# Kernel optimization log

Measured on AMD Instinct MI355X. Metric: run time of the kernel, lower is better.

## Reference

```python
import jax, jax.numpy as jnp
import numpy as np
from functools import partial


def conv2d(x, w, b, pad):
    # x: [B,C,H,W], w: [O,I,kh,kw]
    out = jax.lax.conv_general_dilated(
        x, w, window_strides=(1, 1), padding=[(pad, pad), (pad, pad)],
        dimension_numbers=("NCHW", "OIHW", "NCHW"))
    return out + b[None, :, None, None]


def maxpool3x3_s1(x):
    return jax.lax.reduce_window(
        x, -jnp.inf, jax.lax.max, (1, 1, 3, 3), (1, 1, 1, 1),
        padding=((0, 0), (0, 0), (1, 1), (1, 1)))


def bilinear_sample(img, y, x):
    # img: [B,C,H,W]; y, x: [B,H,W] float sample coords. Zero outside bounds.
    def one(im, yy, xx):  # im [C,H,W]
        H, W = im.shape[1], im.shape[2]
        y0 = jnp.floor(yy)
        x0 = jnp.floor(xx)
        wy = yy - y0
        wx = xx - x0
        y0i = y0.astype(jnp.int32)
        x0i = x0.astype(jnp.int32)

        def g(yi, xi):
            valid = (yi >= 0) & (yi < H) & (xi >= 0) & (xi < W)
            yc = jnp.clip(yi, 0, H - 1)
            xc = jnp.clip(xi, 0, W - 1)
            return im[:, yc, xc] * valid[None].astype(im.dtype)

        return (g(y0i, x0i) * ((1 - wy) * (1 - wx))[None]
                + g(y0i, x0i + 1) * ((1 - wy) * wx)[None]
                + g(y0i + 1, x0i) * (wy * (1 - wx))[None]
                + g(y0i + 1, x0i + 1) * (wy * wx)[None])

    return jax.vmap(one)(img, y, x)


def deform_conv2d(x, offset, weight, bias, k, pad):
    # torchvision-style: offset [B, 2*k*k, H, W], pairs are (dy, dx) in
    # row-major kernel order. stride=1, dilation=1.
    B, C, H, W = x.shape
    off = offset.reshape(B, k * k, 2, H, W)
    hh = jnp.arange(H, dtype=x.dtype)[None, :, None]  # [1,H,1]
    ww = jnp.arange(W, dtype=x.dtype)[None, None, :]  # [1,1,W]
    out = jnp.zeros((B, weight.shape[0], H, W), x.dtype)
    for t in range(k * k):
        i, j = t // k, t % k
        y = hh + (i - pad) + off[:, t, 0]  # [B,H,W]
        xc = ww + (j - pad) + off[:, t, 1]
        s = bilinear_sample(x, y, xc)      # [B,C,H,W]
        out = out + jnp.einsum("bchw,oc->bohw", s, weight[:, :, i, j])
    return out + bias[None, :, None, None]


def _mk(key, shape, scale=0.05):
    return jax.random.normal(key, shape, dtype=jnp.float32) * scale


def setup_inputs() -> dict:
    key = jax.random.key(0)
    ks = jax.random.split(key, 20)
    C = 512
    Cb = C // 4  # 128
    B, H, W = 8, 64, 64
    return {
        "x": jax.random.normal(ks[0], (B, C, H, W), dtype=jnp.float32),
        "w_b1": _mk(ks[1], (Cb, C, 1, 1)), "b_b1": jnp.zeros((Cb,), jnp.float32),
        "w_b21": _mk(ks[2], (Cb, C, 1, 1)), "b_b21": jnp.zeros((Cb,), jnp.float32),
        "w_off2": _mk(ks[3], (18, Cb, 3, 3), 0.01), "b_off2": jnp.zeros((18,), jnp.float32),
        "w_ddc2": _mk(ks[4], (Cb, Cb, 3, 3)), "b_ddc2": jnp.zeros((Cb,), jnp.float32),
        "w_b31": _mk(ks[5], (Cb, C, 1, 1)), "b_b31": jnp.zeros((Cb,), jnp.float32),
        "w_off3": _mk(ks[6], (50, Cb, 5, 5), 0.01), "b_off3": jnp.zeros((50,), jnp.float32),
        "w_ddc3": _mk(ks[7], (Cb, Cb, 5, 5)), "b_ddc3": jnp.zeros((Cb,), jnp.float32),
        "w_b4": _mk(ks[8], (Cb, C, 1, 1)), "b_b4": jnp.zeros((Cb,), jnp.float32),
        "w_cc": _mk(ks[9], (C, Cb * 4, 1, 1)), "b_cc": jnp.zeros((C,), jnp.float32),
    }


def reference(x, w_b1, b_b1, w_b21, b_b21, w_off2, b_off2, w_ddc2, b_ddc2,
              w_b31, b_b31, w_off3, b_off3, w_ddc3, b_ddc3, w_b4, b_b4,
              w_cc, b_cc):
    b1 = conv2d(x, w_b1, b_b1, 0)

    b2i = conv2d(x, w_b21, b_b21, 0)
    off2 = conv2d(b2i, w_off2, b_off2, 1)
    b2 = deform_conv2d(b2i, off2, w_ddc2, b_ddc2, k=3, pad=1)

    b3i = conv2d(x, w_b31, b_b31, 0)
    off3 = conv2d(b3i, w_off3, b_off3, 2)
    b3 = deform_conv2d(b3i, off3, w_ddc3, b_ddc3, k=5, pad=2)

    b4 = conv2d(maxpool3x3_s1(x), w_b4, b_b4, 0)

    cat = jnp.concatenate([b1, b2, b3, b4], axis=1) * x
    fused = conv2d(cat, w_cc, b_cc, 0)
    return x + jax.nn.sigmoid(fused)
```

## Files before the change

### kernel.cpp

```cpp
#include <hip/hip_runtime.h>
#include <math.h>

#define HW 4096
typedef short short8 __attribute__((ext_vector_type(8)));
typedef float floatx4 __attribute__((ext_vector_type(4)));

#define O_XBT   0ull
#define O_PXB   33554432ull
#define O_CATB  67108864ull
#define O_WPB   100663296ull
#define O_W4B   101056512ull
#define O_WCCB  101187584ull
#define O_WD2T  101711872ull
#define O_WD3T  102006784ull
#define O_WO2T  102825984ull
#define O_WO3T  102973440ull
#define O_T2B   33554432ull
#define O_T3B   41943040ull
#define O_OFF2  50331648ull
#define O_OFF3  52690944ull

__device__ __forceinline__ unsigned short f2b(float f) {
    union { float f; unsigned u; } v; v.f = f;
    unsigned r = v.u + 0x7FFFu + ((v.u >> 16) & 1u);
    return (unsigned short)(r >> 16);
}
__device__ __forceinline__ float lou(unsigned u) {
    union { unsigned u; float f; } v; v.u = u << 16; return v.f;
}
__device__ __forceinline__ float hiu(unsigned u) {
    union { unsigned u; float f; } v; v.u = u & 0xFFFF0000u; return v.f;
}
__device__ __forceinline__ unsigned pk2(float lo, float hi) {
    return (unsigned)f2b(lo) | ((unsigned)f2b(hi) << 16);
}

__global__ __launch_bounds__(256) void k_prepw(
        const float* __restrict__ w1, const float* __restrict__ w21,
        const float* __restrict__ w31, const float* __restrict__ w4,
        const float* __restrict__ wcc, const float* __restrict__ wd2,
        const float* __restrict__ wd3, const float* __restrict__ wo2,
        const float* __restrict__ wo3, unsigned short* __restrict__ ws8) {
    unsigned i = blockIdx.x * 256 + threadIdx.x;
    unsigned short* wpb  = ws8 + (O_WPB  >> 1);
    unsigned short* w4b  = ws8 + (O_W4B  >> 1);
    unsigned short* wccb = ws8 + (O_WCCB >> 1);
    unsigned short* wd2t = ws8 + (O_WD2T >> 1);
    unsigned short* wd3t = ws8 + (O_WD3T >> 1);
    unsigned short* wo2t = ws8 + (O_WO2T >> 1);
    unsigned short* wo3t = ws8 + (O_WO3T >> 1);
    if (i < 196608) {
        int o = i >> 9;
        float v = (o < 128) ? w1[i] : (o < 256) ? w21[i - 65536] : w31[i - 131072];
        wpb[i] = f2b(v);
    } else if (i < 262144) {
        unsigned j = i - 196608; w4b[j] = f2b(w4[j]);
    } else if (i < 524288) {
        unsigned j = i - 262144; wccb[j] = f2b(wcc[j]);
    } else if (i < 671744) {
        unsigned j = i - 524288; int t = j >> 14, o = (j >> 7) & 127, c = j & 127;
        wd2t[j] = f2b(wd2[((o * 128 + c) * 9) + t]);
    } else if (i < 1081344) {
        unsigned j = i - 671744; int t = j >> 14, o = (j >> 7) & 127, c = j & 127;
        wd3t[j] = f2b(wd3[((o * 128 + c) * 25) + t]);
    } else if (i < 1155072) {
        unsigned j = i - 1081344; int t = j >> 13, o = (j >> 7) & 63, c = j & 127;
        wo2t[j] = (o < 18) ? f2b(wo2[((o * 128 + c) * 9) + t]) : 0;
    } else if (i < 1359872) {
        unsigned j = i - 1155072; int t = j >> 13, o = (j >> 7) & 63, c = j & 127;
        wo3t[j] = (o < 50) ? f2b(wo3[((o * 128 + c) * 25) + t]) : 0;
    }
}

__global__ __launch_bounds__(256) void k_xpose(const float* __restrict__ X,
                                               unsigned short* __restrict__ xbT) {
    __shared__ unsigned short t[32][33];
    const int p0 = blockIdx.x * 32, c0 = blockIdx.y * 32, b = blockIdx.z;
    const int tid = threadIdx.x;
    #pragma unroll
    for (int s = 0; s < 4; ++s) {
        int cl = s * 8 + (tid >> 5), pl = tid & 31;
        t[cl][pl] = f2b(X[((size_t)b * 512 + c0 + cl) * HW + p0 + pl]);
    }
    __syncthreads();
    #pragma unroll
    for (int s = 0; s < 4; ++s) {
        int pl = s * 8 + (tid >> 5), cl = tid & 31;
        xbT[((size_t)b * HW + p0 + pl) * 512 + c0 + cl] = t[cl][pl];
    }
}

__global__ __launch_bounds__(256) void k_pool(const unsigned short* __restrict__ xbT,
                                              unsigned short* __restrict__ pxb) {
    unsigned gid = blockIdx.x * 256 + threadIdx.x;
    int b = gid >> 18;
    unsigned rem = gid & 262143;
    int pos = rem >> 6;
    int cg = (rem & 63) * 8;
    int h = pos >> 6, w = pos & 63;
    const unsigned short* img = xbT + (size_t)b * HW * 512;
    float m[8] = {-INFINITY, -INFINITY, -INFINITY, -INFINITY,
                  -INFINITY, -INFINITY, -INFINITY, -INFINITY};
    #pragma unroll
    for (int dy = -1; dy <= 1; ++dy) {
        int hh = h + dy;
        if (hh < 0 || hh >= 64) continue;
        #pragma unroll
        for (int dx = -1; dx <= 1; ++dx) {
            int ww = w + dx;
            if (ww < 0 || ww >= 64) continue;
            uint4 v = *(const uint4*)(img + ((size_t)(hh * 64 + ww)) * 512 + cg);
            unsigned uu[4] = {v.x, v.y, v.z, v.w};
            #pragma unroll
            for (int e = 0; e < 4; ++e) {
                m[2 * e]     = fmaxf(m[2 * e],     lou(uu[e]));
                m[2 * e + 1] = fmaxf(m[2 * e + 1], hiu(uu[e]));
            }
        }
    }
    uint4 o;
    o.x = pk2(m[0], m[1]); o.y = pk2(m[2], m[3]);
    o.z = pk2(m[4], m[5]); o.w = pk2(m[6], m[7]);
    *(uint4*)(pxb + ((size_t)b * HW + pos) * 512 + cg) = o;
}

#define SA(r,c) SM[(r)*40 + (c)]
#define SB(r,c) SM[5120 + (r)*40 + (c)]
#define SC(r,c) SM[(r)*136 + (c)]
__global__ __launch_bounds__(256) void k_gemm(
        const unsigned short* __restrict__ A, const float* __restrict__ bias,
        const unsigned short* __restrict__ Bm,
        unsigned short* __restrict__ dst, int dStride, int dOff) {
    __shared__ unsigned short SM[17408];
    const int tid = threadIdx.x;
    const int n0 = blockIdx.x * 128;
    const int b = blockIdx.z;
    const int wave = tid >> 6, lane = tid & 63, quad = lane >> 4, lr = lane & 15;
    const int m0w = (wave & 1) * 64, n0w = (wave >> 1) * 64;
    const int srow = tid >> 1, skh = (tid & 1) * 16;
    floatx4 acc[4][4] = {};

    for (int k0 = 0; k0 < 512; k0 += 32) {
        const unsigned short* ga = A + (size_t)srow * 512 + k0 + skh;
        uint4 a0 = *(const uint4*)(ga);
        uint4 a1 = *(const uint4*)(ga + 8);
        const unsigned short* gb = Bm + ((size_t)b * HW + n0 + srow) * 512 + k0 + skh;
        uint4 b0 = *(const uint4*)(gb);
        uint4 b1 = *(const uint4*)(gb + 8);
        __syncthreads();
        *(uint4*)&SA(srow, skh) = a0;
        *(uint4*)&SA(srow, skh + 8) = a1;
        *(uint4*)&SB(srow, skh) = b0;
        *(uint4*)&SB(srow, skh + 8) = b1;
        __syncthreads();
        short8 af[4], bf[4];
        #pragma unroll
        for (int i = 0; i < 4; ++i) af[i] = *(short8*)&SA(m0w + i * 16 + lr, quad * 8);
        #pragma unroll
        for (int j = 0; j < 4; ++j) bf[j] = *(short8*)&SB(n0w + j * 16 + lr, quad * 8);
        #pragma unroll
        for (int i = 0; i < 4; ++i)
            #pragma unroll
            for (int j = 0; j < 4; ++j)
                acc[i][j] = __builtin_amdgcn_mfma_f32_16x16x32_bf16(af[i], bf[j], acc[i][j], 0, 0, 0);
    }
    __syncthreads();
    #pragma unroll
    for (int i = 0; i < 4; ++i) {
        float4 bs = *(const float4*)&bias[m0w + i * 16 + quad * 4];
        #pragma unroll
        for (int j = 0; j < 4; ++j) {
            floatx4 v = acc[i][j];
            int pos = n0w + j * 16 + lr;
            int ch = m0w + i * 16 + quad * 4;
            uint2 st;
            st.x = pk2(v[0] + bs.x, v[1] + bs.y);
            st.y = pk2(v[2] + bs.z, v[3] + bs.w);
            *(uint2*)&SC(pos, ch) = st;
        }
    }
    __syncthreads();
    #pragma unroll
    for (int r = 0; r < 8; ++r) {
        int pos = (tid >> 4) + r * 16;
        *(uint4*)&dst[((size_t)b * HW + n0 + pos) * dStride + dOff + (tid & 15) * 8] =
            *(uint4*)&SC(pos, (tid & 15) * 8);
    }
}

template<int KS, int OCH>
__global__ __launch_bounds__(512) void k_offconv2(
        const unsigned short* __restrict__ img,
        const unsigned short* __restrict__ woT,
        const float* __restrict__ bias, float* __restrict__ Out) {
    constexpr int PAD = KS / 2;
    constexpr int TT = KS * KS;
    constexpr int SR = 2 + 2 * PAD;
    constexpr int SC2 = 64 + 2 * PAD;
    constexpr int NE = SR * SC2;
    __shared__ unsigned short slab[NE * 36];
    __shared__ float ctile[64 * 132];
    const int tid = threadIdx.x;
    const int p0 = blockIdx.x * 128, hrow0 = blockIdx.x * 2, b = blockIdx.z;
    const int wave = tid >> 6, lane = tid & 63, quad = lane >> 4, lr = lane & 15;
    const int wm = wave & 1, wn = wave >> 1;
    const unsigned short* ib = img + (size_t)b * HW * 128;
    floatx4 acc[2][2] = {};

    for (int c0 = 0; c0 < 128; c0 += 32) {
        __syncthreads();
        if (tid < NE) {
            int s = tid / SC2, cl = tid % SC2;
            int r = hrow0 - PAD + s, cc = cl - PAD;
            uint4 v0 = {}, v1 = {}, v2 = {}, v3 = {};
            if ((unsigned)r < 64u && (unsigned)cc < 64u) {
                const uint4* g = (const uint4*)(ib + ((size_t)(r * 64 + cc)) * 128 + c0);
                v0 = g[0]; v1 = g[1]; v2 = g[2]; v3 = g[3];
            }
            uint2* d2 = (uint2*)&slab[tid * 36];
            d2[0] = make_uint2(v0.x, v0.y); d2[1] = make_uint2(v0.z, v0.w);
            d2[2] = make_uint2(v1.x, v1.y); d2[3] = make_uint2(v1.z, v1.w);
            d2[4] = make_uint2(v2.x, v2.y); d2[5] = make_uint2(v2.z, v2.w);
            d2[6] = make_uint2(v3.x, v3.y); d2[7] = make_uint2(v3.z, v3.w);
        }
        __syncthreads();
        #pragma unroll
        for (int t = 0; t < TT; ++t) {
            const int ky = t / KS, kx = t % KS;
            short8 af[2], bf[2];
            #pragma unroll
            for (int i = 0; i < 2; ++i)
                af[i] = *(const short8*)&woT[((size_t)t * 64 + wm * 32 + i * 16 + lr) * 128
                                             + c0 + quad * 8];
            #pragma unroll
            for (int j = 0; j < 2; ++j) {
                int p = wn * 32 + j * 16 + lr;
                int e = ((p >> 6) + ky) * SC2 + (p & 63) + kx;
                union { uint2 u[2]; short8 s; } bb;
                const uint2* sp = (const uint2*)&slab[e * 36 + quad * 8];
                bb.u[0] = sp[0]; bb.u[1] = sp[1];
                bf[j] = bb.s;
            }
            #pragma unroll
            for (int i = 0; i < 2; ++i)
                #pragma unroll
                for (int j = 0; j < 2; ++j)
                    acc[i][j] = __builtin_amdgcn_mfma_f32_16x16x32_bf16(af[i], bf[j], acc[i][j], 0, 0, 0);
        }
    }
    __syncthreads();
    #pragma unroll
    for (int i = 0; i < 2; ++i)
        #pragma unroll
        for (int j = 0; j < 2; ++j) {
            floatx4 v = acc[i][j];
            int p = wn * 32 + j * 16 + lr;
            int o = wm * 32 + i * 16 + quad * 4;
            #pragma unroll
            for (int rg = 0; rg < 4; ++rg)
                ctile[(o + rg) * 132 + p] = v[rg];
        }
    __syncthreads();
    {
        int o = tid >> 3, seg = tid & 7;
        if (o < OCH) {
            float bs = bias[o];
            const float* src = &ctile[o * 132 + seg * 16];
            float* dst = &Out[((size_t)b * OCH + o) * HW + p0 + seg * 16];
            #pragma unroll
            for (int q = 0; q < 4; ++q) {
                float4 v = *(const float4*)(src + q * 4);
                v.x += bs; v.y += bs; v.z += bs; v.w += bs;
                *(float4*)(dst + q * 4) = v;
            }
        }
    }
}

template<int KS>
__global__ __launch_bounds__(512, 4) void k_deform7(
        const unsigned short* __restrict__ img,
        const float* __restrict__ Off,
        const unsigned short* __restrict__ wdT,
        const float* __restrict__ bias,
        unsigned short* __restrict__ catb, int dOff) {
    constexpr int PAD = KS / 2;
    constexpr int TT = KS * KS;
    __shared__ unsigned short sS[64][136];
    const int tid = threadIdx.x;
    const int b = blockIdx.z;
    const int p0 = blockIdx.x * 64;
    const int wave = tid >> 6, lane = tid & 63, quad = lane >> 4, lr = lane & 15;
    const int m0w = (wave & 3) * 32;
    const int n0w = (wave >> 2) * 32;
    const int pos = tid >> 3;
    const int cseg = (tid & 7) * 16;
    const int pglob = p0 + pos;
    const int h = blockIdx.x, w = pos;
    const unsigned short* ib = img + (size_t)b * HW * 128;
    const float* offb = Off + (size_t)b * 2 * TT * HW;
    floatx4 acc[2][2] = {};

    for (int t = 0; t < TT; ++t) {
        float dy = offb[(size_t)(2 * t) * HW + pglob];
        float dx = offb[(size_t)(2 * t + 1) * HW + pglob];
        float fy = (float)(h + t / KS - PAD) + dy;
        float fx = (float)(w + t % KS - PAD) + dx;
        float y0f = floorf(fy), x0f = floorf(fx);
        float wy = fy - y0f, wx = fx - x0f;
        int y0 = (int)y0f, x0 = (int)x0f;
        float w00 = (1.f - wy) * (1.f - wx), w01 = (1.f - wy) * wx;
        float w10 = wy * (1.f - wx), w11 = wy * wx;
        bool yv0 = (unsigned)y0 < 64u, yv1 = (unsigned)(y0 + 1) < 64u;
        bool xv0 = (unsigned)x0 < 64u, xv1 = (unsigned)(x0 + 1) < 64u;
        uint4 cA[2] = {}, cB[2] = {}, cC[2] = {}, cD[2] = {};
        long bidx = (long)(y0 * 64 + x0) * 128 + cseg;
        if (yv0 && xv0) { const uint4* p = (const uint4*)(ib + bidx);
            cA[0] = p[0]; cA[1] = p[1]; }
        if (yv0 && xv1) { const uint4* p = (const uint4*)(ib + bidx + 128);
            cB[0] = p[0]; cB[1] = p[1]; }
        if (yv1 && xv0) { const uint4* p = (const uint4*)(ib + bidx + 8192);
            cC[0] = p[0]; cC[1] = p[1]; }
        if (yv1 && xv1) { const uint4* p = (const uint4*)(ib + bidx + 8320);
            cD[0] = p[0]; cD[1] = p[1]; }
        uint4 outv[2];
        #pragma unroll
        for (int j = 0; j < 2; ++j) {
            unsigned a[4] = {cA[j].x, cA[j].y, cA[j].z, cA[j].w};
            unsigned bb[4] = {cB[j].x, cB[j].y, cB[j].z, cB[j].w};
            unsigned c[4] = {cC[j].x, cC[j].y, cC[j].z, cC[j].w};
            unsigned d[4] = {cD[j].x, cD[j].y, cD[j].z, cD[j].w};
            unsigned r[4];
            #pragma unroll
            for (int e = 0; e < 4; ++e) {
                float lo = w00 * lou(a[e]) + w01 * lou(bb[e]) + w10 * lou(c[e]) + w11 * lou(d[e]);
                float hi = w00 * hiu(a[e]) + w01 * hiu(bb[e]) + w10 * hiu(c[e]) + w11 * hiu(d[e]);
                r[e] = pk2(lo, hi);
            }
            outv[j].x = r[0]; outv[j].y = r[1]; outv[j].z = r[2]; outv[j].w = r[3];
        }
        __syncthreads();
        *(uint4*)&sS[pos][cseg] = outv[0];
        *(uint4*)&sS[pos][cseg + 8] = outv[1];
        __syncthreads();
        const unsigned short* wt = wdT + (size_t)t * 128 * 128;
        #pragma unroll
        for (int ks = 0; ks < 4; ++ks) {
            short8 af[2], bf[2];
            #pragma unroll
            for (int i = 0; i < 2; ++i)
                af[i] = *(const short8*)&wt[(size_t)(m0w + i * 16 + lr) * 128
                                            + ks * 32 + quad * 8];
            #pragma unroll
            for (int j = 0; j < 2; ++j)
                bf[j] = *(short8*)&sS[n0w + j * 16 + lr][ks * 32 + quad * 8];
            #pragma unroll
            for (int i = 0; i < 2; ++i)
                #pragma unroll
                for (int j = 0; j < 2; ++j)
                    acc[i][j] = __builtin_amdgcn_mfma_f32_16x16x32_bf16(af[i], bf[j], acc[i][j], 0, 0, 0);
        }
    }
    __syncthreads();
    #pragma unroll
    for (int i = 0; i < 2; ++i) {
        float4 bs = *(const float4*)&bias[m0w + i * 16 + quad * 4];
        #pragma unroll
        for (int j = 0; j < 2; ++j) {
            floatx4 v = acc[i][j];
            int p = n0w + j * 16 + lr;
            int ch = m0w + i * 16 + quad * 4;
            uint2 st;
            st.x = pk2(v[0] + bs.x, v[1] + bs.y);
            st.y = pk2(v[2] + bs.z, v[3] + bs.w);
            *(uint2*)&sS[p][ch] = st;
        }
    }
    __syncthreads();
    #pragma unroll
    for (int r = 0; r < 2; ++r) {
        int idx = r * 512 + tid;
        int p = idx >> 4, sg = (idx & 15) * 8;
        *(uint4*)&catb[((size_t)b * HW + p0 + p) * 512 + dOff + sg] =
            *(uint4*)&sS[p][sg];
    }
}

__global__ __launch_bounds__(256) void k_gemm_final(
        const unsigned short* __restrict__ A, const float* __restrict__ bias,
        const unsigned short* __restrict__ catb, const unsigned short* __restrict__ xbT,
        const float* __restrict__ X, float* __restrict__ OutF) {
    __shared__ unsigned short sA[128][40];
    __shared__ unsigned short sB[128][40];
    const int tid = threadIdx.x;
    const int n0 = blockIdx.x * 128;
    const int o0 = blockIdx.y * 128;
    const int b = blockIdx.z;
    const int wave = tid >> 6, lane = tid & 63, quad = lane >> 4, lr = lane & 15;
    const int m0w = (wave & 1) * 64, n0w = (wave >> 1) * 64;
    const int srow = tid >> 1, skh = (tid & 1) * 16;
    floatx4 acc[4][4] = {};

    for (int k0 = 0; k0 < 512; k0 += 32) {
        const unsigned short* ga = A + (size_t)(o0 + srow) * 512 + k0 + skh;
        uint4 a0 = *(const uint4*)(ga);
        uint4 a1 = *(const uint4*)(ga + 8);
        size_t bi = ((size_t)b * HW + n0 + srow) * 512 + k0 + skh;
        uint4 c0 = *(const uint4*)(catb + bi);
        uint4 c1 = *(const uint4*)(catb + bi + 8);
        uint4 x0 = *(const uint4*)(xbT + bi);
        uint4 x1 = *(const uint4*)(xbT + bi + 8);
        unsigned cu[8] = {c0.x, c0.y, c0.z, c0.w, c1.x, c1.y, c1.z, c1.w};
        unsigned xu[8] = {x0.x, x0.y, x0.z, x0.w, x1.x, x1.y, x1.z, x1.w};
        unsigned mu[8];
        #pragma unroll
        for (int e = 0; e < 8; ++e)
            mu[e] = pk2(lou(cu[e]) * lou(xu[e]), hiu(cu[e]) * hiu(xu[e]));
        __syncthreads();
        *(uint4*)&sA[srow][skh] = a0;
        *(uint4*)&sA[srow][skh + 8] = a1;
        uint4 m0v; m0v.x = mu[0]; m0v.y = mu[1]; m0v.z = mu[2]; m0v.w = mu[3];
        uint4 m1v; m1v.x = mu[4]; m1v.y = mu[5]; m1v.z = mu[6]; m1v.w = mu[7];
        *(uint4*)&sB[srow][skh] = m0v;
        *(uint4*)&sB[srow][skh + 8] = m1v;
        __syncthreads();
        short8 af[4], bf[4];
        #pragma unroll
        for (int i = 0; i < 4; ++i) af[i] = *(short8*)&sA[m0w + i * 16 + lr][quad * 8];
        #pragma unroll
        for (int j = 0; j < 4; ++j) bf[j] = *(short8*)&sB[n0w + j * 16 + lr][quad * 8];
        #pragma unroll
        for (int i = 0; i < 4; ++i)
            #pragma unroll
            for (int j = 0; j < 4; ++j)
                acc[i][j] = __builtin_amdgcn_mfma_f32_16x16x32_bf16(af[i], bf[j], acc[i][j], 0, 0, 0);
    }
    #pragma unroll
    for (int i = 0; i < 4; ++i) {
        float4 bs = *(const float4*)&bias[o0 + m0w + i * 16 + quad * 4];
        float bsa[4] = {bs.x, bs.y, bs.z, bs.w};
        #pragma unroll
        for (int j = 0; j < 4; ++j) {
            floatx4 v = acc[i][j];
            int pos = n0 + n0w + j * 16 + lr;
            #pragma unroll
            for (int rg = 0; rg < 4; ++rg) {
                int o = o0 + m0w + i * 16 + quad * 4 + rg;
                float f = v[rg] + bsa[rg];
                float sg = 1.f / (1.f + __expf(-f));
                size_t idx = ((size_t)b * 512 + o) * HW + pos;
                OutF[idx] = X[idx] + sg;
            }
        }
    }
}

extern "C" void kernel_launch(void* const* d_in, const int* in_sizes, int n_in,
                              void* d_out, int out_size, void* d_ws, size_t ws_size,
                              hipStream_t stream) {
    const float* x      = (const float*)d_in[0];
    const float* w_b1   = (const float*)d_in[1];
    const float* b_b1   = (const float*)d_in[2];
    const float* w_b21  = (const float*)d_in[3];
    const float* b_b21  = (const float*)d_in[4];
    const float* w_off2 = (const float*)d_in[5];
    const float* b_off2 = (const float*)d_in[6];
    const float* w_ddc2 = (const float*)d_in[7];
    const float* b_ddc2 = (const float*)d_in[8];
    const float* w_b31  = (const float*)d_in[9];
    const float* b_b31  = (const float*)d_in[10];
    const float* w_off3 = (const float*)d_in[11];
    const float* b_off3 = (const float*)d_in[12];
    const float* w_ddc3 = (const float*)d_in[13];
    const float* b_ddc3 = (const float*)d_in[14];
    const float* w_b4   = (const float*)d_in[15];
    const float* b_b4   = (const float*)d_in[16];
    const float* w_cc   = (const float*)d_in[17];
    const float* b_cc   = (const float*)d_in[18];

    char* wsb = (char*)d_ws;
    unsigned short* ws8  = (unsigned short*)d_ws;
    unsigned short* xbT  = (unsigned short*)(wsb + O_XBT);
    unsigned short* pxb  = (unsigned short*)(wsb + O_PXB);
    unsigned short* catb = (unsigned short*)(wsb + O_CATB);
    unsigned short* wpb  = (unsigned short*)(wsb + O_WPB);
    unsigned short* w4b  = (unsigned short*)(wsb + O_W4B);
    unsigned short* wccb = (unsigned short*)(wsb + O_WCCB);
    unsigned short* wd2t = (unsigned short*)(wsb + O_WD2T);
    unsigned short* wd3t = (unsigned short*)(wsb + O_WD3T);
    unsigned short* wo2t = (unsigned short*)(wsb + O_WO2T);
    unsigned short* wo3t = (unsigned short*)(wsb + O_WO3T);
    unsigned short* t2b  = (unsigned short*)(wsb + O_T2B);
    unsigned short* t3b  = (unsigned short*)(wsb + O_T3B);
    float* off2 = (float*)(wsb + O_OFF2);
    float* off3 = (float*)(wsb + O_OFF3);
    float* out  = (float*)d_out;

    k_prepw<<<dim3(5312), dim3(256), 0, stream>>>(
        w_b1, w_b21, w_b31, w_b4, w_cc, w_ddc2, w_ddc3, w_off2, w_off3, ws8);
    k_xpose<<<dim3(128, 16, 8), dim3(256), 0, stream>>>(x, xbT);
    k_pool<<<dim3(8192), dim3(256), 0, stream>>>(xbT, pxb);
    k_gemm<<<dim3(32, 1, 8), dim3(256), 0, stream>>>(w4b, b_b4, pxb, catb, 512, 384);
    k_gemm<<<dim3(32, 1, 8), dim3(256), 0, stream>>>(wpb, b_b1, xbT, catb, 512, 0);
    k_gemm<<<dim3(32, 1, 8), dim3(256), 0, stream>>>(wpb + 128 * 512, b_b21, xbT, t2b, 128, 0);
    k_gemm<<<dim3(32, 1, 8), dim3(256), 0, stream>>>(wpb + 256 * 512, b_b31, xbT, t3b, 128, 0);
    k_offconv2<3, 18><<<dim3(32, 1, 8), dim3(512), 0, stream>>>(t2b, wo2t, b_off2, off2);
    k_offconv2<5, 50><<<dim3(32, 1, 8), dim3(512), 0, stream>>>(t3b, wo3t, b_off3, off3);
    k_deform7<3><<<dim3(64, 1, 8), dim3(512), 0, stream>>>(t2b, off2, wd2t, b_ddc2, catb, 128);
    k_deform7<5><<<dim3(64, 1, 8), dim3(512), 0, stream>>>(t3b, off3, wd3t, b_ddc3, catb, 256);
    k_gemm_final<<<dim3(32, 4, 8), dim3(256), 0, stream>>>(wccb, b_cc, catb, xbT, x, out);
}
```

Measured before the change: 555.2 us.

## Software-pipeline deform conv gather with double-buffered shared tile

```diff
diff --git a/kernel.cpp b/kernel.cpp
--- a/kernel.cpp
+++ b/kernel.cpp
@@ -277,8 +277,48 @@
     }
 }
 
+#define DC_GATHER(T, DY, DX) do {                                              \
+    float fy = (float)(h + (T) / KS - PAD) + (DY);                             \
+    float fx = (float)(w + (T) % KS - PAD) + (DX);                             \
+    float y0f = floorf(fy), x0f = floorf(fx);                                  \
+    float wyv = fy - y0f, wxv = fx - x0f;                                      \
+    int y0 = (int)y0f, x0 = (int)x0f;                                          \
+    w00 = (1.f - wyv) * (1.f - wxv); w01 = (1.f - wyv) * wxv;                  \
+    w10 = wyv * (1.f - wxv);         w11 = wyv * wxv;                          \
+    bool yv0 = (unsigned)y0 < 64u, yv1 = (unsigned)(y0 + 1) < 64u;             \
+    bool xv0 = (unsigned)x0 < 64u, xv1 = (unsigned)(x0 + 1) < 64u;             \
+    long bidx = (long)(y0 * 64 + x0) * 128 + cseg;                             \
+    cn0 = z4; cn1 = z4; cn2 = z4; cn3 = z4;                                    \
+    cn4 = z4; cn5 = z4; cn6 = z4; cn7 = z4;                                    \
+    if (yv0 && xv0) { const uint4* p_ = (const uint4*)(ib + bidx);             \
+        cn0 = p_[0]; cn1 = p_[1]; }                                            \
+    if (yv0 && xv1) { const uint4* p_ = (const uint4*)(ib + bidx + 128);       \
+        cn2 = p_[0]; cn3 = p_[1]; }                                            \
+    if (yv1 && xv0) { const uint4* p_ = (const uint4*)(ib + bidx + 8192);      \
+        cn4 = p_[0]; cn5 = p_[1]; }                                            \
+    if (yv1 && xv1) { const uint4* p_ = (const uint4*)(ib + bidx + 8320);      \
+        cn6 = p_[0]; cn7 = p_[1]; }                                            \
+} while (0)
+
+#define DC_BLEND(RA, RB, RC, RD, OUT) do {                                     \
+    unsigned a_[4] = {RA.x, RA.y, RA.z, RA.w};                                 \
+    unsigned b_[4] = {RB.x, RB.y, RB.z, RB.w};                                 \
+    unsigned c_[4] = {RC.x, RC.y, RC.z, RC.w};                                 \
+    unsigned d_[4] = {RD.x, RD.y, RD.z, RD.w};                                 \
+    unsigned r_[4];                                                            \
+    _Pragma("unroll")                                                          \
+    for (int e_ = 0; e_ < 4; ++e_) {                                           \
+        float lo_ = w00 * lou(a_[e_]) + w01 * lou(b_[e_])                      \
+                  + w10 * lou(c_[e_]) + w11 * lou(d_[e_]);                     \
+        float hi_ = w00 * hiu(a_[e_]) + w01 * hiu(b_[e_])                      \
+                  + w10 * hiu(c_[e_]) + w11 * hiu(d_[e_]);                     \
+        r_[e_] = pk2(lo_, hi_);                                                \
+    }                                                                          \
+    OUT.x = r_[0]; OUT.y = r_[1]; OUT.z = r_[2]; OUT.w = r_[3];                \
+} while (0)
+
 template<int KS>
-__global__ __launch_bounds__(512, 4) void k_deform7(
+__global__ __launch_bounds__(512, 4) void k_deform8(
         const unsigned short* __restrict__ img,
         const float* __restrict__ Off,
         const unsigned short* __restrict__ wdT,
@@ -286,7 +326,7 @@
         unsigned short* __restrict__ catb, int dOff) {
     constexpr int PAD = KS / 2;
     constexpr int TT = KS * KS;
-    __shared__ unsigned short sS[64][136];
+    __shared__ unsigned short sS[2][64][136];
     const int tid = threadIdx.x;
     const int b = blockIdx.z;
     const int p0 = blockIdx.x * 64;
@@ -299,82 +339,80 @@
     const int h = blockIdx.x, w = pos;
     const unsigned short* ib = img + (size_t)b * HW * 128;
     const float* offb = Off + (size_t)b * 2 * TT * HW;
-    floatx4 acc[2][2] = {};
+    const uint4 z4 = make_uint4(0u, 0u, 0u, 0u);
+
+    floatx4 acc00 = {}, acc01 = {}, acc10 = {}, acc11 = {};
+    uint4 cn0, cn1, cn2, cn3, cn4, cn5, cn6, cn7;
+    float w00, w01, w10, w11;
+    float noy = 0.f, nox = 0.f;
+
+    {
+        float dy0 = offb[pglob];
+        float dx0 = offb[HW + pglob];
+        DC_GATHER(0, dy0, dx0);
+    }
+    if (TT > 1) { noy = offb[2 * HW + pglob]; nox = offb[3 * HW + pglob]; }
 
     for (int t = 0; t < TT; ++t) {
-        float dy = offb[(size_t)(2 * t) * HW + pglob];
-        float dx = offb[(size_t)(2 * t + 1) * HW + pglob];
-        float fy = (float)(h + t / KS - PAD) + dy;
-        float fx = (float)(w + t % KS - PAD) + dx;
-        float y0f = floorf(fy), x0f = floorf(fx);
-        float wy = fy - y0f, wx = fx - x0f;
-        int y0 = (int)y0f, x0 = (int)x0f;
-        float w00 = (1.f - wy) * (1.f - wx), w01 = (1.f - wy) * wx;
-        float w10 = wy * (1.f - wx), w11 = wy * wx;
-        bool yv0 = (unsigned)y0 < 64u, yv1 = (unsigned)(y0 + 1) < 64u;
-        bool xv0 = (unsigned)x0 < 64u, xv1 = (unsigned)(x0 + 1) < 64u;
-        uint4 cA[2] = {}, cB[2] = {}, cC[2] = {}, cD[2] = {};
-        long bidx = (long)(y0 * 64 + x0) * 128 + cseg;
-        if (yv0 && xv0) { const uint4* p = (const uint4*)(ib + bidx);
-            cA[0] = p[0]; cA[1] = p[1]; }
-        if (yv0 && xv1) { const uint4* p = (const uint4*)(ib + bidx + 128);
-            cB[0] = p[0]; cB[1] = p[1]; }
-        if (yv1 && xv0) { const uint4* p = (const uint4*)(ib + bidx + 8192);
-            cC[0] = p[0]; cC[1] = p[1]; }
-        if (yv1 && xv1) { const uint4* p = (const uint4*)(ib + bidx + 8320);
-            cD[0] = p[0]; cD[1] = p[1]; }
-        uint4 outv[2];
-        #pragma unroll
-        for (int j = 0; j < 2; ++j) {
-            unsigned a[4] = {cA[j].x, cA[j].y, cA[j].z, cA[j].w};
-            unsigned bb[4] = {cB[j].x, cB[j].y, cB[j].z, cB[j].w};
-            unsigned c[4] = {cC[j].x, cC[j].y, cC[j].z, cC[j].w};
-            unsigned d[4] = {cD[j].x, cD[j].y, cD[j].z, cD[j].w};
-            unsigned r[4];
-            #pragma unroll
-            for (int e = 0; e < 4; ++e) {
-                float lo = w00 * lou(a[e]) + w01 * lou(bb[e]) + w10 * lou(c[e]) + w11 * lou(d[e]);
-                float hi = w00 * hiu(a[e]) + w01 * hiu(bb[e]) + w10 * hiu(c[e]) + w11 * hiu(d[e]);
-                r[e] = pk2(lo, hi);
+        const int cur = t & 1;
+        uint4 ov0, ov1;
+        DC_BLEND(cn0, cn2, cn4, cn6, ov0);
+        DC_BLEND(cn1, cn3, cn5, cn7, ov1);
+        *(uint4*)&sS[cur][pos][cseg] = ov0;
+        *(uint4*)&sS[cur][pos][cseg + 8] = ov1;
+        __syncthreads();
+        const unsigned short* wb = wdT + (size_t)t * 16384
+                                   + (size_t)(m0w + lr) * 128 + quad * 8;
+        short8 wr0 = *(const short8*)(wb);
+        short8 wr1 = *(const short8*)(wb + 2048);
+        short8 wr2 = *(const short8*)(wb + 32);
+        short8 wr3 = *(const short8*)(wb + 2080);
+        short8 wr4 = *(const short8*)(wb + 64);
+        short8 wr5 = *(const short8*)(wb + 2112);
+        short8 wr6 = *(const short8*)(wb + 96);
+        short8 wr7 = *(const short8*)(wb + 2144);
+        if (t + 1 < TT) {
+            DC_GATHER(t + 1, noy, nox);
+            if (t + 2 < TT) {
+                noy = offb[(size_t)(2 * t + 4) * HW + pglob];
+                nox = offb[(size_t)(2 * t + 5) * HW + pglob];
             }
-            outv[j].x = r[0]; outv[j].y = r[1]; outv[j].z = r[2]; outv[j].w = r[3];
-        }
-        __syncthreads();
-        *(uint4*)&sS[pos][cseg] = outv[0];
-        *(uint4*)&sS[pos][cseg + 8] = outv[1];
-        __syncthreads();
-        const unsigned short* wt = wdT + (size_t)t * 128 * 128;
+        }
         #pragma unroll
         for (int ks = 0; ks < 4; ++ks) {
-            short8 af[2], bf[2];
-            #pragma unroll
-            for (int i = 0; i < 2; ++i)
-                af[i] = *(const short8*)&wt[(size_t)(m0w + i * 16 + lr) * 128
-                                            + ks * 32 + quad * 8];
-            #pragma unroll
-            for (int j = 0; j < 2; ++j)
-                bf[j] = *(short8*)&sS[n0w + j * 16 + lr][ks * 32 + quad * 8];
-            #pragma unroll
-            for (int i = 0; i < 2; ++i)
-                #pragma unroll
-                for (int j = 0; j < 2; ++j)
-                    acc[i][j] = __builtin_amdgcn_mfma_f32_16x16x32_bf16(af[i], bf[j], acc[i][j], 0, 0, 0);
-        }
-    }
-    __syncthreads();
-    #pragma unroll
-    for (int i = 0; i < 2; ++i) {
-        float4 bs = *(const float4*)&bias[m0w + i * 16 + quad * 4];
-        #pragma unroll
-        for (int j = 0; j < 2; ++j) {
-            floatx4 v = acc[i][j];
-            int p = n0w + j * 16 + lr;
-            int ch = m0w + i * 16 + quad * 4;
-            uint2 st;
-            st.x = pk2(v[0] + bs.x, v[1] + bs.y);
-            st.y = pk2(v[2] + bs.z, v[3] + bs.w);
-            *(uint2*)&sS[p][ch] = st;
-        }
+            short8 bf0 = *(short8*)&sS[cur][n0w + lr][ks * 32 + quad * 8];
+            short8 bf1 = *(short8*)&sS[cur][n0w + 16 + lr][ks * 32 + quad * 8];
+            short8 a0 = (ks == 0) ? wr0 : (ks == 1) ? wr2 : (ks == 2) ? wr4 : wr6;
+            short8 a1 = (ks == 0) ? wr1 : (ks == 1) ? wr3 : (ks == 2) ? wr5 : wr7;
+            acc00 = __builtin_amdgcn_mfma_f32_16x16x32_bf16(a0, bf0, acc00, 0, 0, 0);
+            acc01 = __builtin_amdgcn_mfma_f32_16x16x32_bf16(a0, bf1, acc01, 0, 0, 0);
+            acc10 = __builtin_amdgcn_mfma_f32_16x16x32_bf16(a1, bf0, acc10, 0, 0, 0);
+            acc11 = __builtin_amdgcn_mfma_f32_16x16x32_bf16(a1, bf1, acc11, 0, 0, 0);
+        }
+    }
+    __syncthreads();
+    {
+        float4 bs = *(const float4*)&bias[m0w + quad * 4];
+        float4 bs2 = *(const float4*)&bias[m0w + 16 + quad * 4];
+        floatx4 v;
+        uint2 st;
+        int ch0 = m0w + quad * 4, ch1 = m0w + 16 + quad * 4;
+        v = acc00;
+        st.x = pk2(v[0] + bs.x, v[1] + bs.y);
+        st.y = pk2(v[2] + bs.z, v[3] + bs.w);
+        *(uint2*)&sS[0][n0w + lr][ch0] = st;
+        v = acc01;
+        st.x = pk2(v[0] + bs.x, v[1] + bs.y);
+        st.y = pk2(v[2] + bs.z, v[3] + bs.w);
+        *(uint2*)&sS[0][n0w + 16 + lr][ch0] = st;
+        v = acc10;
+        st.x = pk2(v[0] + bs2.x, v[1] + bs2.y);
+        st.y = pk2(v[2] + bs2.z, v[3] + bs2.w);
+        *(uint2*)&sS[0][n0w + lr][ch1] = st;
+        v = acc11;
+        st.x = pk2(v[0] + bs2.x, v[1] + bs2.y);
+        st.y = pk2(v[2] + bs2.z, v[3] + bs2.w);
+        *(uint2*)&sS[0][n0w + 16 + lr][ch1] = st;
     }
     __syncthreads();
     #pragma unroll
@@ -382,7 +420,7 @@
         int idx = r * 512 + tid;
         int p = idx >> 4, sg = (idx & 15) * 8;
         *(uint4*)&catb[((size_t)b * HW + p0 + p) * 512 + dOff + sg] =
-            *(uint4*)&sS[p][sg];
+            *(uint4*)&sS[0][p][sg];
     }
 }
 
@@ -506,7 +544,7 @@
     k_gemm<<<dim3(32, 1, 8), dim3(256), 0, stream>>>(wpb + 256 * 512, b_b31, xbT, t3b, 128, 0);
     k_offconv2<3, 18><<<dim3(32, 1, 8), dim3(512), 0, stream>>>(t2b, wo2t, b_off2, off2);
     k_offconv2<5, 50><<<dim3(32, 1, 8), dim3(512), 0, stream>>>(t3b, wo3t, b_off3, off3);
-    k_deform7<3><<<dim3(64, 1, 8), dim3(512), 0, stream>>>(t2b, off2, wd2t, b_ddc2, catb, 128);
-    k_deform7<5><<<dim3(64, 1, 8), dim3(512), 0, stream>>>(t3b, off3, wd3t, b_ddc3, catb, 256);
+    k_deform8<3><<<dim3(64, 1, 8), dim3(512), 0, stream>>>(t2b, off2, wd2t, b_ddc2, catb, 128);
+    k_deform8<5><<<dim3(64, 1, 8), dim3(512), 0, stream>>>(t3b, off3, wd3t, b_ddc3, catb, 256);
     k_gemm_final<<<dim3(32, 4, 8), dim3(256), 0, stream>>>(wccb, b_cc, catb, xbT, x, out);
 }
```

Result: no change. 554.5 us (-0.1%).
